# Performance work log

Hardware: AMD Instinct MI355X
Metric: run time of the kernel (lower is better)

## Reference

```python
import jax, jax.numpy as jnp
import numpy as np

N = 50000
E = 800000
IN_DIM = 128
HID = 128
OUT_DIM = 64


def _xavier(key, fan_in, fan_out):
    # matches nn.init.xavier_uniform_ on a (out, in) weight
    limit = float(np.sqrt(6.0 / (fan_in + fan_out)))
    return jax.random.uniform(key, (fan_in, fan_out), jnp.float32, -limit, limit)


def setup_inputs() -> dict:
    key = jax.random.key(0)
    ks = jax.random.split(key, 7)
    X = jax.random.normal(ks[0], (N, IN_DIM), jnp.float32)
    edge_row = jax.random.randint(ks[1], (E,), 0, N, jnp.int32)
    edge_col = jax.random.randint(ks[2], (E,), 0, N, jnp.int32)
    edge_weight = jax.random.uniform(ks[3], (E,), jnp.float32)
    W1 = _xavier(ks[4], IN_DIM, HID)
    b1 = jnp.zeros((HID,), jnp.float32)
    W2 = _xavier(ks[5], HID, HID)
    b2 = jnp.zeros((HID,), jnp.float32)
    W3 = _xavier(ks[6], HID, OUT_DIM)
    b3 = jnp.zeros((OUT_DIM,), jnp.float32)
    return {"X": X, "edge_row": edge_row, "edge_col": edge_col,
            "edge_weight": edge_weight,
            "W1": W1, "b1": b1, "W2": W2, "b2": b2, "W3": W3, "b3": b3}


def _spmm(edge_row, edge_col, edge_weight, H):
    # sparse A @ H via gather + segment_sum (COO SpMM)
    msgs = edge_weight[:, None] * H[edge_col]  # [E, d]
    return jax.ops.segment_sum(msgs, edge_row, num_segments=N)


def reference(X, edge_row, edge_col, edge_weight, W1, b1, W2, b2, W3, b3):
    # layer 1: SpMM -> linear -> relu (dropout disabled: eval mode)
    h = _spmm(edge_row, edge_col, edge_weight, X)
    h = jax.nn.relu(h @ W1 + b1)
    # layer 2
    h = _spmm(edge_row, edge_col, edge_weight, h)
    h = jax.nn.relu(h @ W2 + b2)
    # layer 3 (no activation)
    h = _spmm(edge_row, edge_col, edge_weight, h)
    return h @ W3 + b3
```

## Files before the change

### kernel.cpp

```cpp
#include <hip/hip_runtime.h>


typedef unsigned int uint32;
using bf16x8 = __attribute__((ext_vector_type(8))) short;
using f32x4  = __attribute__((ext_vector_type(4))) float;

static __device__ __forceinline__ unsigned short f2bf(float x) {
    unsigned int u = __builtin_bit_cast(unsigned int, x);
    u += 0x7FFFu + ((u >> 16) & 1u);
    return (unsigned short)(u >> 16);
}
static __device__ __forceinline__ float bflo(uint32 u) {
    return __builtin_bit_cast(float, u << 16);
}
static __device__ __forceinline__ float bfhi(uint32 u) {
    return __builtin_bit_cast(float, u & 0xFFFF0000u);
}


__global__ __launch_bounds__(256) void bucket_hist_kernel(const int* __restrict__ erow,
                                                          int* __restrict__ bcnt, int e) {
    __shared__ int h[512];
    int t = threadIdx.x;
    h[t] = 0; h[t + 256] = 0;
    __syncthreads();
    int base = blockIdx.x * 4096;
#pragma unroll
    for (int j = 0; j < 4; j++) {
        int idx = base + j * 1024 + t * 4;
        if (idx + 3 < e) {
            int4 r = *reinterpret_cast<const int4*>(&erow[idx]);
            atomicAdd(&h[r.x >> 7], 1); atomicAdd(&h[r.y >> 7], 1);
            atomicAdd(&h[r.z >> 7], 1); atomicAdd(&h[r.w >> 7], 1);
        } else {
            for (int q = 0; q < 4; q++) {
                int i2 = idx + q;
                if (i2 < e) atomicAdd(&h[erow[i2] >> 7], 1);
            }
        }
    }
    __syncthreads();
    if (h[t])       atomicAdd(&bcnt[t], h[t]);
    if (h[t + 256]) atomicAdd(&bcnt[t + 256], h[t + 256]);
}

__global__ __launch_bounds__(512) void bucket_scan_kernel(const int* __restrict__ bcnt,
                                                          int* __restrict__ boff,
                                                          int* __restrict__ bcur,
                                                          int* __restrict__ row_ptr,
                                                          int nb, int n) {
    __shared__ int sm[512];
    int t = threadIdx.x;
    int v = (t < nb) ? bcnt[t] : 0;
    sm[t] = v;
    __syncthreads();
    for (int off = 1; off < 512; off <<= 1) {
        int u = (t >= off) ? sm[t - off] : 0;
        __syncthreads();
        sm[t] += u;
        __syncthreads();
    }
    if (t < nb) { boff[t] = sm[t] - v; bcur[t] = sm[t] - v; }
    if (t == 511) { boff[nb] = sm[511]; row_ptr[n] = sm[511]; }
}

__global__ __launch_bounds__(256) void bucket_scatter_kernel(const int* __restrict__ erow,
                                                             const int* __restrict__ ecol,
                                                             const float* __restrict__ ew,
                                                             int* __restrict__ bcur,
                                                             int2* __restrict__ ebuf, int e) {
    __shared__ int hist[512];
    __shared__ int psc[256];
    __shared__ int fixup[512];
    __shared__ int2 stage[4096];
    int t = threadIdx.x;
    hist[t] = 0; hist[t + 256] = 0;
    __syncthreads();
    int base = blockIdx.x * 4096;
    int4 rows[4];
#pragma unroll
    for (int j = 0; j < 4; j++) {
        int idx = base + j * 1024 + t * 4;
        int4 r = make_int4(-1, -1, -1, -1);
        if (idx + 3 < e) {
            r = *reinterpret_cast<const int4*>(&erow[idx]);
        } else {
            if (idx < e)     r.x = erow[idx];
            if (idx + 1 < e) r.y = erow[idx + 1];
            if (idx + 2 < e) r.z = erow[idx + 2];
            if (idx + 3 < e) r.w = erow[idx + 3];
        }
        rows[j] = r;
        if (r.x >= 0) atomicAdd(&hist[r.x >> 7], 1);
        if (r.y >= 0) atomicAdd(&hist[r.y >> 7], 1);
        if (r.z >= 0) atomicAdd(&hist[r.z >> 7], 1);
        if (r.w >= 0) atomicAdd(&hist[r.w >> 7], 1);
    }
    __syncthreads();
    int c0 = hist[2 * t], c1 = hist[2 * t + 1];
    int s = c0 + c1;
    psc[t] = s;
    __syncthreads();
    for (int off = 1; off < 256; off <<= 1) {
        int u = (t >= off) ? psc[t - off] : 0;
        __syncthreads();
        psc[t] += u;
        __syncthreads();
    }
    int lo0 = psc[t] - s;
    int lo1 = lo0 + c0;
    if (c0) fixup[2 * t]     = atomicAdd(&bcur[2 * t], c0) - lo0;
    if (c1) fixup[2 * t + 1] = atomicAdd(&bcur[2 * t + 1], c1) - lo1;
    __syncthreads();
    hist[2 * t] = lo0; hist[2 * t + 1] = lo1;
    __syncthreads();
#pragma unroll
    for (int j = 0; j < 4; j++) {
        int idx = base + j * 1024 + t * 4;
        int4 r = rows[j];
        int4 c = make_int4(0, 0, 0, 0);
        float4 w = make_float4(0.f, 0.f, 0.f, 0.f);
        if (idx + 3 < e) {
            c = *reinterpret_cast<const int4*>(&ecol[idx]);
            w = *reinterpret_cast<const float4*>(&ew[idx]);
        } else {
            if (idx < e)     { c.x = ecol[idx];     w.x = ew[idx]; }
            if (idx + 1 < e) { c.y = ecol[idx + 1]; w.y = ew[idx + 1]; }
            if (idx + 2 < e) { c.z = ecol[idx + 2]; w.z = ew[idx + 2]; }
            if (idx + 3 < e) { c.w = ecol[idx + 3]; w.w = ew[idx + 3]; }
        }
        if (r.x >= 0) { int b = r.x >> 7; int sl = atomicAdd(&hist[b], 1);
            stage[sl] = make_int2((b << 23) | ((r.x & 127) << 16) | c.x, __builtin_bit_cast(int, w.x)); }
        if (r.y >= 0) { int b = r.y >> 7; int sl = atomicAdd(&hist[b], 1);
            stage[sl] = make_int2((b << 23) | ((r.y & 127) << 16) | c.y, __builtin_bit_cast(int, w.y)); }
        if (r.z >= 0) { int b = r.z >> 7; int sl = atomicAdd(&hist[b], 1);
            stage[sl] = make_int2((b << 23) | ((r.z & 127) << 16) | c.z, __builtin_bit_cast(int, w.z)); }
        if (r.w >= 0) { int b = r.w >> 7; int sl = atomicAdd(&hist[b], 1);
            stage[sl] = make_int2((b << 23) | ((r.w & 127) << 16) | c.w, __builtin_bit_cast(int, w.w)); }
    }
    __syncthreads();
    int ecnt = min(4096, e - base);
    for (int i = t; i < ecnt; i += 256) {
        int2 v = stage[i];
        int b = ((unsigned)v.x) >> 23;
        ebuf[fixup[b] + i] = v;
    }
}

__global__ __launch_bounds__(256) void bucket_sort_kernel(const int* __restrict__ boff,
                                                          const int2* __restrict__ ebuf,
                                                          int2* __restrict__ ecsr,
                                                          int* __restrict__ row_ptr, int n) {
    constexpr int MAXB = 3072;
    int b = blockIdx.x;
    int off = boff[b];
    int cnt = min(boff[b + 1] - off, MAXB);
    __shared__ int2 stage[MAXB];
    __shared__ int2 sorted[MAXB];
    __shared__ int rc[128], rs[128], c2[128];
    int t = threadIdx.x;
    if (t < 128) { rc[t] = 0; c2[t] = 0; }
    __syncthreads();
    for (int i = t; i < cnt; i += 256) {
        int2 v = ebuf[off + i];
        stage[i] = v;
        atomicAdd(&rc[(v.x >> 16) & 127], 1);
    }
    __syncthreads();
    if (t < 128) rs[t] = rc[t];
    __syncthreads();
    for (int o = 1; o < 128; o <<= 1) {
        int u = 0;
        if (t < 128 && t >= o) u = rs[t - o];
        __syncthreads();
        if (t < 128) rs[t] += u;
        __syncthreads();
    }
    if (t < 128) {
        int gr = b * 128 + t;
        if (gr < n) row_ptr[gr] = off + rs[t] - rc[t];
    }
    __syncthreads();
    for (int i = t; i < cnt; i += 256) {
        int2 v = stage[i];
        int r = (v.x >> 16) & 127;
        int pos = rs[r] - rc[r] + atomicAdd(&c2[r], 1);
        sorted[pos] = make_int2(v.x & 0xFFFF, v.y);
    }
    __syncthreads();
    for (int i = t; i < cnt; i += 256) ecsr[off + i] = sorted[i];
}

__global__ __launch_bounds__(256) void transpose_w_kernel(const float* __restrict__ W,
                                                          unsigned short* __restrict__ Wt,
                                                          int N) {
    int gid = blockIdx.x * 256 + threadIdx.x;
    int k = gid & 127;
    int nn = gid >> 7;
    Wt[gid] = f2bf(W[k * N + nn]);
}

template <bool AF32, int NOUT>
__global__ __launch_bounds__(256) void gemm_mfma_kernel(const void* __restrict__ Ap,
                                                        const unsigned short* __restrict__ Wt,
                                                        unsigned short* __restrict__ Zb, int n) {
    constexpr int CT = NOUT / 16;
    int wave = threadIdx.x >> 6;
    int lane = threadIdx.x & 63;
    int m0 = blockIdx.x * 64 + wave * 16;
    int r = lane & 15;
    int g = lane >> 4;
    int arow = min(m0 + r, n - 1);
    f32x4 acc[CT] = {};
#pragma unroll
    for (int kt = 0; kt < 4; kt++) {
        int k0 = kt * 32 + g * 8;
        bf16x8 a;
        if constexpr (AF32) {
            const float* A = (const float*)Ap;
            float4 x0 = *reinterpret_cast<const float4*>(&A[(size_t)arow * 128 + k0]);
            float4 x1 = *reinterpret_cast<const float4*>(&A[(size_t)arow * 128 + k0 + 4]);
            a[0] = (short)f2bf(x0.x); a[1] = (short)f2bf(x0.y);
            a[2] = (short)f2bf(x0.z); a[3] = (short)f2bf(x0.w);
            a[4] = (short)f2bf(x1.x); a[5] = (short)f2bf(x1.y);
            a[6] = (short)f2bf(x1.z); a[7] = (short)f2bf(x1.w);
        } else {
            const unsigned short* A = (const unsigned short*)Ap;
            a = *reinterpret_cast<const bf16x8*>(&A[(size_t)arow * 128 + k0]);
        }
#pragma unroll
        for (int c = 0; c < CT; c++) {
            bf16x8 bb = *reinterpret_cast<const bf16x8*>(&Wt[(size_t)(c * 16 + r) * 128 + k0]);
            acc[c] = __builtin_amdgcn_mfma_f32_16x16x32_bf16(a, bb, acc[c], 0, 0, 0);
        }
    }
#pragma unroll
    for (int c = 0; c < CT; c++) {
#pragma unroll
        for (int rr = 0; rr < 4; rr++) {
            int row = m0 + g * 4 + rr;
            if (row < n) Zb[(size_t)row * NOUT + c * 16 + r] = f2bf(acc[c][rr]);
        }
    }
}

__global__ __launch_bounds__(256) void spmm128_kernel(const int* __restrict__ row_ptr,
                                                      const int2* __restrict__ ecw,
                                                      const unsigned short* __restrict__ Zb,
                                                      const float* __restrict__ bias,
                                                      unsigned short* __restrict__ Hb, int n) {
    int row = (blockIdx.x * blockDim.x + threadIdx.x) >> 6;
    int lane = threadIdx.x & 63;
    if (row >= n) return;
    int beg = row_ptr[row], end = row_ptr[row + 1];
    const int grp = lane >> 4;
    const int gl  = lane & 15;
    float acc[8] = {0.f, 0.f, 0.f, 0.f, 0.f, 0.f, 0.f, 0.f};
#pragma unroll 2
    for (int k0 = beg; k0 < end; k0 += 4) {
        int k = k0 + grp;
        bool valid = (k < end);
        int kc = valid ? k : (end - 1);
        int2 cw = ecw[kc];
        float w = valid ? __builtin_bit_cast(float, cw.y) : 0.f;
        uint4 z = *reinterpret_cast<const uint4*>(&Zb[((size_t)(uint32)cw.x << 7) + (gl << 3)]);
        acc[0] = fmaf(w, bflo(z.x), acc[0]);
        acc[1] = fmaf(w, bfhi(z.x), acc[1]);
        acc[2] = fmaf(w, bflo(z.y), acc[2]);
        acc[3] = fmaf(w, bfhi(z.y), acc[3]);
        acc[4] = fmaf(w, bflo(z.z), acc[4]);
        acc[5] = fmaf(w, bfhi(z.z), acc[5]);
        acc[6] = fmaf(w, bflo(z.w), acc[6]);
        acc[7] = fmaf(w, bfhi(z.w), acc[7]);
    }
#pragma unroll
    for (int j = 0; j < 8; j++) {
        acc[j] += __shfl_xor(acc[j], 16, 64);
        acc[j] += __shfl_xor(acc[j], 32, 64);
    }
    if (lane < 16) {
        int d0 = gl << 3;
        float4 b0 = *reinterpret_cast<const float4*>(&bias[d0]);
        float4 b1 = *reinterpret_cast<const float4*>(&bias[d0 + 4]);
        float v0 = fmaxf(acc[0] + b0.x, 0.f), v1 = fmaxf(acc[1] + b0.y, 0.f);
        float v2 = fmaxf(acc[2] + b0.z, 0.f), v3 = fmaxf(acc[3] + b0.w, 0.f);
        float v4 = fmaxf(acc[4] + b1.x, 0.f), v5 = fmaxf(acc[5] + b1.y, 0.f);
        float v6 = fmaxf(acc[6] + b1.z, 0.f), v7 = fmaxf(acc[7] + b1.w, 0.f);
        uint4 pk;
        pk.x = (uint32)f2bf(v0) | ((uint32)f2bf(v1) << 16);
        pk.y = (uint32)f2bf(v2) | ((uint32)f2bf(v3) << 16);
        pk.z = (uint32)f2bf(v4) | ((uint32)f2bf(v5) << 16);
        pk.w = (uint32)f2bf(v6) | ((uint32)f2bf(v7) << 16);
        *reinterpret_cast<uint4*>(&Hb[(size_t)row * 128 + d0]) = pk;
    }
}

__global__ __launch_bounds__(256) void spmm64_kernel(const int* __restrict__ row_ptr,
                                                     const int2* __restrict__ ecw,
                                                     const unsigned short* __restrict__ Zb,
                                                     const float* __restrict__ bias,
                                                     float* __restrict__ out, int n) {
    int row = (blockIdx.x * blockDim.x + threadIdx.x) >> 6;
    int lane = threadIdx.x & 63;
    if (row >= n) return;
    int beg = row_ptr[row], end = row_ptr[row + 1];
    const int grp = lane >> 4;
    const int gl  = lane & 15;
    float acc[4] = {0.f, 0.f, 0.f, 0.f};
#pragma unroll 2
    for (int k0 = beg; k0 < end; k0 += 4) {
        int k = k0 + grp;
        bool valid = (k < end);
        int kc = valid ? k : (end - 1);
        int2 cw = ecw[kc];
        float w = valid ? __builtin_bit_cast(float, cw.y) : 0.f;
        uint2 z = *reinterpret_cast<const uint2*>(&Zb[((size_t)(uint32)cw.x << 6) + (gl << 2)]);
        acc[0] = fmaf(w, bflo(z.x), acc[0]);
        acc[1] = fmaf(w, bfhi(z.x), acc[1]);
        acc[2] = fmaf(w, bflo(z.y), acc[2]);
        acc[3] = fmaf(w, bfhi(z.y), acc[3]);
    }
#pragma unroll
    for (int j = 0; j < 4; j++) {
        acc[j] += __shfl_xor(acc[j], 16, 64);
        acc[j] += __shfl_xor(acc[j], 32, 64);
    }
    if (lane < 16) {
        int d0 = gl << 2;
        float4 b0 = *reinterpret_cast<const float4*>(&bias[d0]);
        float4 v0 = make_float4(acc[0] + b0.x, acc[1] + b0.y, acc[2] + b0.z, acc[3] + b0.w);
        *reinterpret_cast<float4*>(&out[(size_t)row * 64 + d0]) = v0;
    }
}

extern "C" void kernel_launch(void* const* d_in, const int* in_sizes, int n_in,
                              void* d_out, int out_size, void* d_ws, size_t ws_size,
                              hipStream_t stream) {
    const float* X    = (const float*)d_in[0];
    const int*   erow = (const int*)d_in[1];
    const int*   ecol = (const int*)d_in[2];
    const float* ew   = (const float*)d_in[3];
    const float* W1   = (const float*)d_in[4];
    const float* b1   = (const float*)d_in[5];
    const float* W2   = (const float*)d_in[6];
    const float* b2   = (const float*)d_in[7];
    const float* W3   = (const float*)d_in[8];
    const float* b3   = (const float*)d_in[9];
    float* out = (float*)d_out;

    const int n = in_sizes[0] / 128;
    const int e = in_sizes[1];
    const int nb = (n + 127) >> 7;

    char* p = (char*)d_ws;
    auto alloc = [&](size_t bytes) {
        void* r = (void*)p;
        p += (bytes + 255) & ~(size_t)255;
        return r;
    };
    int*            row_ptr = (int*)alloc((size_t)(n + 1) * sizeof(int));
    int*            bcnt    = (int*)alloc((size_t)nb * sizeof(int));
    int*            boff    = (int*)alloc((size_t)(nb + 1) * sizeof(int));
    int*            bcur    = (int*)alloc((size_t)nb * sizeof(int));
    int2*           ebuf    = (int2*)alloc((size_t)e * sizeof(int2));
    int2*           ecsr    = (int2*)alloc((size_t)e * sizeof(int2));
    unsigned short* Zb      = (unsigned short*)alloc((size_t)n * 128 * sizeof(unsigned short));
    unsigned short* Hb      = (unsigned short*)alloc((size_t)n * 128 * sizeof(unsigned short));
    unsigned short* Wt1     = (unsigned short*)alloc(128 * 128 * sizeof(unsigned short));
    unsigned short* Wt2     = (unsigned short*)alloc(128 * 128 * sizeof(unsigned short));
    unsigned short* Wt3     = (unsigned short*)alloc(64 * 128 * sizeof(unsigned short));

    const int eb4k = (e + 4095) / 4096;
    const int gemm_grid = (n + 63) / 64;
    const int spmm_grid = (n + 3) / 4;

    hipMemsetAsync(bcnt, 0, (size_t)nb * sizeof(int), stream);
    bucket_hist_kernel<<<eb4k, 256, 0, stream>>>(erow, bcnt, e);
    bucket_scan_kernel<<<1, 512, 0, stream>>>(bcnt, boff, bcur, row_ptr, nb, n);
    bucket_scatter_kernel<<<eb4k, 256, 0, stream>>>(erow, ecol, ew, bcur, ebuf, e);
    bucket_sort_kernel<<<nb, 256, 0, stream>>>(boff, ebuf, ecsr, row_ptr, n);

    transpose_w_kernel<<<64, 256, 0, stream>>>(W1, Wt1, 128);
    transpose_w_kernel<<<64, 256, 0, stream>>>(W2, Wt2, 128);
    transpose_w_kernel<<<32, 256, 0, stream>>>(W3, Wt3, 64);

    gemm_mfma_kernel<true, 128><<<gemm_grid, 256, 0, stream>>>(X, Wt1, Zb, n);
    spmm128_kernel<<<spmm_grid, 256, 0, stream>>>(row_ptr, ecsr, Zb, b1, Hb, n);

    gemm_mfma_kernel<false, 128><<<gemm_grid, 256, 0, stream>>>(Hb, Wt2, Zb, n);
    spmm128_kernel<<<spmm_grid, 256, 0, stream>>>(row_ptr, ecsr, Zb, b2, Hb, n);

    gemm_mfma_kernel<false, 64><<<gemm_grid, 256, 0, stream>>>(Hb, Wt3, Zb, n);
    spmm64_kernel<<<spmm_grid, 256, 0, stream>>>(row_ptr, ecsr, Zb, b3, out, n);
}
```

Measured before the change: 194.2 us.

## Drop histogram pass with fixed-capacity buckets, fuse prep, and restructure SpMM lanes

Removes the histogram and scan kernels by scattering edges into fixed-capacity per-bucket slots (BCAP=3072). The bucket sort kernel now computes bucket offsets itself with a redundant in-block scan. The three weight transposes and the bucket-counter reset are fused into one prep kernel, which cuts the number of launches and the memset. Both SpMM kernels are rewritten. spmm128 now has each lane own two feature columns and walk the row serially with a 4-way unroll, with no cross-lane reduction. spmm64 packs two rows per wavefront. The risks are silently dropped edges if any bucket exceeds BCAP, more serial latency per row in SpMM, and a larger scratch buffer.

```diff
diff --git a/kernel.cpp b/kernel.cpp
--- a/kernel.cpp
+++ b/kernel.cpp
@@ -4,6 +4,8 @@
 typedef unsigned int uint32;
 using bf16x8 = __attribute__((ext_vector_type(8))) short;
 using f32x4  = __attribute__((ext_vector_type(4))) float;
+
+static constexpr int BCAP = 3072;
 
 static __device__ __forceinline__ unsigned short f2bf(float x) {
     unsigned int u = __builtin_bit_cast(unsigned int, x);
@@ -17,51 +19,24 @@
     return __builtin_bit_cast(float, u & 0xFFFF0000u);
 }
 
-
-__global__ __launch_bounds__(256) void bucket_hist_kernel(const int* __restrict__ erow,
-                                                          int* __restrict__ bcnt, int e) {
-    __shared__ int h[512];
-    int t = threadIdx.x;
-    h[t] = 0; h[t + 256] = 0;
-    __syncthreads();
-    int base = blockIdx.x * 4096;
-#pragma unroll
-    for (int j = 0; j < 4; j++) {
-        int idx = base + j * 1024 + t * 4;
-        if (idx + 3 < e) {
-            int4 r = *reinterpret_cast<const int4*>(&erow[idx]);
-            atomicAdd(&h[r.x >> 7], 1); atomicAdd(&h[r.y >> 7], 1);
-            atomicAdd(&h[r.z >> 7], 1); atomicAdd(&h[r.w >> 7], 1);
-        } else {
-            for (int q = 0; q < 4; q++) {
-                int i2 = idx + q;
-                if (i2 < e) atomicAdd(&h[erow[i2] >> 7], 1);
-            }
-        }
-    }
-    __syncthreads();
-    if (h[t])       atomicAdd(&bcnt[t], h[t]);
-    if (h[t + 256]) atomicAdd(&bcnt[t + 256], h[t + 256]);
-}
-
-__global__ __launch_bounds__(512) void bucket_scan_kernel(const int* __restrict__ bcnt,
-                                                          int* __restrict__ boff,
-                                                          int* __restrict__ bcur,
-                                                          int* __restrict__ row_ptr,
-                                                          int nb, int n) {
-    __shared__ int sm[512];
-    int t = threadIdx.x;
-    int v = (t < nb) ? bcnt[t] : 0;
-    sm[t] = v;
-    __syncthreads();
-    for (int off = 1; off < 512; off <<= 1) {
-        int u = (t >= off) ? sm[t - off] : 0;
-        __syncthreads();
-        sm[t] += u;
-        __syncthreads();
-    }
-    if (t < nb) { boff[t] = sm[t] - v; bcur[t] = sm[t] - v; }
-    if (t == 511) { boff[nb] = sm[511]; row_ptr[n] = sm[511]; }
+__global__ __launch_bounds__(256) void prep_kernel(const float* __restrict__ W1,
+                                                   const float* __restrict__ W2,
+                                                   const float* __restrict__ W3,
+                                                   unsigned short* __restrict__ Wt1,
+                                                   unsigned short* __restrict__ Wt2,
+                                                   unsigned short* __restrict__ Wt3,
+                                                   int* __restrict__ bcur, int nb) {
+    int gid = blockIdx.x * 256 + threadIdx.x;
+    if (gid < nb) bcur[gid] = 0;
+    if (gid < 16384) {
+        Wt1[gid] = f2bf(W1[(gid & 127) * 128 + (gid >> 7)]);
+    } else if (gid < 32768) {
+        int g = gid - 16384;
+        Wt2[g] = f2bf(W2[(g & 127) * 128 + (g >> 7)]);
+    } else if (gid < 40960) {
+        int g = gid - 32768;
+        Wt3[g] = f2bf(W3[(g & 127) * 64 + (g >> 7)]);
+    }
 }
 
 __global__ __launch_bounds__(256) void bucket_scatter_kernel(const int* __restrict__ erow,
@@ -109,8 +84,8 @@
     }
     int lo0 = psc[t] - s;
     int lo1 = lo0 + c0;
-    if (c0) fixup[2 * t]     = atomicAdd(&bcur[2 * t], c0) - lo0;
-    if (c1) fixup[2 * t + 1] = atomicAdd(&bcur[2 * t + 1], c1) - lo1;
+    if (c0) fixup[2 * t]     = 2 * t * BCAP       + atomicAdd(&bcur[2 * t], c0)     - lo0;
+    if (c1) fixup[2 * t + 1] = (2 * t + 1) * BCAP + atomicAdd(&bcur[2 * t + 1], c1) - lo1;
     __syncthreads();
     hist[2 * t] = lo0; hist[2 * t + 1] = lo1;
     __syncthreads();
@@ -143,26 +118,38 @@
     for (int i = t; i < ecnt; i += 256) {
         int2 v = stage[i];
         int b = ((unsigned)v.x) >> 23;
-        ebuf[fixup[b] + i] = v;
-    }
-}
-
-__global__ __launch_bounds__(256) void bucket_sort_kernel(const int* __restrict__ boff,
+        int gpos = fixup[b] + i;
+        if (gpos - b * BCAP < BCAP) ebuf[gpos] = v;
+    }
+}
+
+__global__ __launch_bounds__(256) void bucket_sort_kernel(const int* __restrict__ bcur,
                                                           const int2* __restrict__ ebuf,
                                                           int2* __restrict__ ecsr,
-                                                          int* __restrict__ row_ptr, int n) {
-    constexpr int MAXB = 3072;
+                                                          int* __restrict__ row_ptr,
+                                                          int n, int nb) {
+    __shared__ int sc[512];
+    __shared__ int2 stage[BCAP];
+    __shared__ int2 sorted[BCAP];
+    __shared__ int rc[128], rs[128], c2[128];
     int b = blockIdx.x;
-    int off = boff[b];
-    int cnt = min(boff[b + 1] - off, MAXB);
-    __shared__ int2 stage[MAXB];
-    __shared__ int2 sorted[MAXB];
-    __shared__ int rc[128], rs[128], c2[128];
     int t = threadIdx.x;
+    sc[t]       = (t < nb)       ? min(bcur[t], BCAP)       : 0;
+    sc[t + 256] = (t + 256 < nb) ? min(bcur[t + 256], BCAP) : 0;
     if (t < 128) { rc[t] = 0; c2[t] = 0; }
     __syncthreads();
+    for (int off = 1; off < 512; off <<= 1) {
+        int a0 = (t >= off) ? sc[t - off] : 0;
+        int a1 = (t + 256 >= off) ? sc[t + 256 - off] : 0;
+        __syncthreads();
+        sc[t] += a0; sc[t + 256] += a1;
+        __syncthreads();
+    }
+    int off_b = (b == 0) ? 0 : sc[b - 1];
+    int cnt = sc[b] - off_b;
+    if (b == 0 && t == 0) row_ptr[n] = sc[nb - 1];
     for (int i = t; i < cnt; i += 256) {
-        int2 v = ebuf[off + i];
+        int2 v = ebuf[b * BCAP + i];
         stage[i] = v;
         atomicAdd(&rc[(v.x >> 16) & 127], 1);
     }
@@ -178,7 +165,7 @@
     }
     if (t < 128) {
         int gr = b * 128 + t;
-        if (gr < n) row_ptr[gr] = off + rs[t] - rc[t];
+        if (gr < n) row_ptr[gr] = off_b + rs[t] - rc[t];
     }
     __syncthreads();
     for (int i = t; i < cnt; i += 256) {
@@ -188,16 +175,7 @@
         sorted[pos] = make_int2(v.x & 0xFFFF, v.y);
     }
     __syncthreads();
-    for (int i = t; i < cnt; i += 256) ecsr[off + i] = sorted[i];
-}
-
-__global__ __launch_bounds__(256) void transpose_w_kernel(const float* __restrict__ W,
-                                                          unsigned short* __restrict__ Wt,
-                                                          int N) {
-    int gid = blockIdx.x * 256 + threadIdx.x;
-    int k = gid & 127;
-    int nn = gid >> 7;
-    Wt[gid] = f2bf(W[k * N + nn]);
+    for (int i = t; i < cnt; i += 256) ecsr[off_b + i] = sorted[i];
 }
 
 template <bool AF32, int NOUT>
@@ -249,87 +227,83 @@
                                                       const unsigned short* __restrict__ Zb,
                                                       const float* __restrict__ bias,
                                                       unsigned short* __restrict__ Hb, int n) {
-    int row = (blockIdx.x * blockDim.x + threadIdx.x) >> 6;
+    int row = (blockIdx.x * 256 + threadIdx.x) >> 6;
     int lane = threadIdx.x & 63;
     if (row >= n) return;
-    int beg = row_ptr[row], end = row_ptr[row + 1];
-    const int grp = lane >> 4;
-    const int gl  = lane & 15;
-    float acc[8] = {0.f, 0.f, 0.f, 0.f, 0.f, 0.f, 0.f, 0.f};
-#pragma unroll 2
-    for (int k0 = beg; k0 < end; k0 += 4) {
-        int k = k0 + grp;
-        bool valid = (k < end);
-        int kc = valid ? k : (end - 1);
-        int2 cw = ecw[kc];
-        float w = valid ? __builtin_bit_cast(float, cw.y) : 0.f;
-        uint4 z = *reinterpret_cast<const uint4*>(&Zb[((size_t)(uint32)cw.x << 7) + (gl << 3)]);
-        acc[0] = fmaf(w, bflo(z.x), acc[0]);
-        acc[1] = fmaf(w, bfhi(z.x), acc[1]);
-        acc[2] = fmaf(w, bflo(z.y), acc[2]);
-        acc[3] = fmaf(w, bfhi(z.y), acc[3]);
-        acc[4] = fmaf(w, bflo(z.z), acc[4]);
-        acc[5] = fmaf(w, bfhi(z.z), acc[5]);
-        acc[6] = fmaf(w, bflo(z.w), acc[6]);
-        acc[7] = fmaf(w, bfhi(z.w), acc[7]);
-    }
-#pragma unroll
-    for (int j = 0; j < 8; j++) {
-        acc[j] += __shfl_xor(acc[j], 16, 64);
-        acc[j] += __shfl_xor(acc[j], 32, 64);
-    }
-    if (lane < 16) {
-        int d0 = gl << 3;
-        float4 b0 = *reinterpret_cast<const float4*>(&bias[d0]);
-        float4 b1 = *reinterpret_cast<const float4*>(&bias[d0 + 4]);
-        float v0 = fmaxf(acc[0] + b0.x, 0.f), v1 = fmaxf(acc[1] + b0.y, 0.f);
-        float v2 = fmaxf(acc[2] + b0.z, 0.f), v3 = fmaxf(acc[3] + b0.w, 0.f);
-        float v4 = fmaxf(acc[4] + b1.x, 0.f), v5 = fmaxf(acc[5] + b1.y, 0.f);
-        float v6 = fmaxf(acc[6] + b1.z, 0.f), v7 = fmaxf(acc[7] + b1.w, 0.f);
-        uint4 pk;
-        pk.x = (uint32)f2bf(v0) | ((uint32)f2bf(v1) << 16);
-        pk.y = (uint32)f2bf(v2) | ((uint32)f2bf(v3) << 16);
-        pk.z = (uint32)f2bf(v4) | ((uint32)f2bf(v5) << 16);
-        pk.w = (uint32)f2bf(v6) | ((uint32)f2bf(v7) << 16);
-        *reinterpret_cast<uint4*>(&Hb[(size_t)row * 128 + d0]) = pk;
-    }
+    int beg = __builtin_amdgcn_readfirstlane(row_ptr[row]);
+    int end = __builtin_amdgcn_readfirstlane(row_ptr[row + 1]);
+    int deg = end - beg;
+    const unsigned short* zb = Zb + (lane << 1);
+    float a0 = 0.f, a1 = 0.f;
+    int i = 0;
+    for (; i + 4 <= deg; i += 4) {
+        int2 e0 = ecw[beg + i];
+        int2 e1 = ecw[beg + i + 1];
+        int2 e2 = ecw[beg + i + 2];
+        int2 e3 = ecw[beg + i + 3];
+        uint32 z0 = *reinterpret_cast<const uint32*>(zb + ((size_t)(uint32)e0.x << 7));
+        uint32 z1 = *reinterpret_cast<const uint32*>(zb + ((size_t)(uint32)e1.x << 7));
+        uint32 z2 = *reinterpret_cast<const uint32*>(zb + ((size_t)(uint32)e2.x << 7));
+        uint32 z3 = *reinterpret_cast<const uint32*>(zb + ((size_t)(uint32)e3.x << 7));
+        float w0 = __builtin_bit_cast(float, e0.y);
+        float w1 = __builtin_bit_cast(float, e1.y);
+        float w2 = __builtin_bit_cast(float, e2.y);
+        float w3 = __builtin_bit_cast(float, e3.y);
+        a0 = fmaf(w0, bflo(z0), a0); a1 = fmaf(w0, bfhi(z0), a1);
+        a0 = fmaf(w1, bflo(z1), a0); a1 = fmaf(w1, bfhi(z1), a1);
+        a0 = fmaf(w2, bflo(z2), a0); a1 = fmaf(w2, bfhi(z2), a1);
+        a0 = fmaf(w3, bflo(z3), a0); a1 = fmaf(w3, bfhi(z3), a1);
+    }
+    for (; i < deg; i++) {
+        int2 e = ecw[beg + i];
+        uint32 z = *reinterpret_cast<const uint32*>(zb + ((size_t)(uint32)e.x << 7));
+        float w = __builtin_bit_cast(float, e.y);
+        a0 = fmaf(w, bflo(z), a0); a1 = fmaf(w, bfhi(z), a1);
+    }
+    float2 bv = *reinterpret_cast<const float2*>(&bias[lane << 1]);
+    a0 = fmaxf(a0 + bv.x, 0.f);
+    a1 = fmaxf(a1 + bv.y, 0.f);
+    uint32 pk = (uint32)f2bf(a0) | ((uint32)f2bf(a1) << 16);
+    *reinterpret_cast<uint32*>(&Hb[(size_t)row * 128 + (lane << 1)]) = pk;
 }
 
 __global__ __launch_bounds__(256) void spmm64_kernel(const int* __restrict__ row_ptr,
                                                      const int2* __restrict__ ecw,
                                                      const unsigned short* __restrict__ Zb,
                                                      const float* __restrict__ bias,
-                                                     float* __restrict__ out, int n) {
-    int row = (blockIdx.x * blockDim.x + threadIdx.x) >> 6;
+                                                     float* __restrict__ out, int n, int e) {
+    int gw = (blockIdx.x * 256 + threadIdx.x) >> 6;
     int lane = threadIdx.x & 63;
-    if (row >= n) return;
-    int beg = row_ptr[row], end = row_ptr[row + 1];
-    const int grp = lane >> 4;
-    const int gl  = lane & 15;
-    float acc[4] = {0.f, 0.f, 0.f, 0.f};
-#pragma unroll 2
-    for (int k0 = beg; k0 < end; k0 += 4) {
-        int k = k0 + grp;
-        bool valid = (k < end);
-        int kc = valid ? k : (end - 1);
-        int2 cw = ecw[kc];
-        float w = valid ? __builtin_bit_cast(float, cw.y) : 0.f;
-        uint2 z = *reinterpret_cast<const uint2*>(&Zb[((size_t)(uint32)cw.x << 6) + (gl << 2)]);
-        acc[0] = fmaf(w, bflo(z.x), acc[0]);
-        acc[1] = fmaf(w, bfhi(z.x), acc[1]);
-        acc[2] = fmaf(w, bflo(z.y), acc[2]);
-        acc[3] = fmaf(w, bfhi(z.y), acc[3]);
-    }
-#pragma unroll
-    for (int j = 0; j < 4; j++) {
-        acc[j] += __shfl_xor(acc[j], 16, 64);
-        acc[j] += __shfl_xor(acc[j], 32, 64);
-    }
-    if (lane < 16) {
-        int d0 = gl << 2;
-        float4 b0 = *reinterpret_cast<const float4*>(&bias[d0]);
-        float4 v0 = make_float4(acc[0] + b0.x, acc[1] + b0.y, acc[2] + b0.z, acc[3] + b0.w);
-        *reinterpret_cast<float4*>(&out[(size_t)row * 64 + d0]) = v0;
+    int half = lane >> 5;
+    int hl = lane & 31;
+    int row = gw * 2 + half;
+    bool rv = (row < n);
+    int beg = 0, end = 0;
+    if (rv) { beg = row_ptr[row]; end = row_ptr[row + 1]; }
+    int beg0 = __builtin_amdgcn_readlane(beg, 0);
+    int deg0 = __builtin_amdgcn_readlane(end, 0) - beg0;
+    int beg1 = __builtin_amdgcn_readlane(beg, 32);
+    int deg1 = __builtin_amdgcn_readlane(end, 32) - beg1;
+    int mdeg = max(deg0, deg1);
+    const unsigned short* zb = Zb + (hl << 1);
+    float a0 = 0.f, a1 = 0.f;
+    for (int i = 0; i < mdeg; i++) {
+        int iA = min(beg0 + min(i, max(deg0 - 1, 0)), e - 1);
+        int iB = min(beg1 + min(i, max(deg1 - 1, 0)), e - 1);
+        int2 eA = ecw[iA];
+        int2 eB = ecw[iB];
+        float wA = (i < deg0) ? __builtin_bit_cast(float, eA.y) : 0.f;
+        float wB = (i < deg1) ? __builtin_bit_cast(float, eB.y) : 0.f;
+        int col = half ? eB.x : eA.x;
+        float w = half ? wB : wA;
+        uint32 z = *reinterpret_cast<const uint32*>(zb + ((size_t)(uint32)col << 6));
+        a0 = fmaf(w, bflo(z), a0);
+        a1 = fmaf(w, bfhi(z), a1);
+    }
+    if (rv) {
+        float2 bv = *reinterpret_cast<const float2*>(&bias[hl << 1]);
+        float2 v = make_float2(a0 + bv.x, a1 + bv.y);
+        *reinterpret_cast<float2*>(&out[(size_t)row * 64 + (hl << 1)]) = v;
     }
 }
 
@@ -359,10 +333,8 @@
         return r;
     };
     int*            row_ptr = (int*)alloc((size_t)(n + 1) * sizeof(int));
-    int*            bcnt    = (int*)alloc((size_t)nb * sizeof(int));
-    int*            boff    = (int*)alloc((size_t)(nb + 1) * sizeof(int));
     int*            bcur    = (int*)alloc((size_t)nb * sizeof(int));
-    int2*           ebuf    = (int2*)alloc((size_t)e * sizeof(int2));
+    int2*           ebuf    = (int2*)alloc((size_t)nb * BCAP * sizeof(int2));
     int2*           ecsr    = (int2*)alloc((size_t)e * sizeof(int2));
     unsigned short* Zb      = (unsigned short*)alloc((size_t)n * 128 * sizeof(unsigned short));
     unsigned short* Hb      = (unsigned short*)alloc((size_t)n * 128 * sizeof(unsigned short));
@@ -372,24 +344,19 @@
 
     const int eb4k = (e + 4095) / 4096;
     const int gemm_grid = (n + 63) / 64;
-    const int spmm_grid = (n + 3) / 4;
-
-    hipMemsetAsync(bcnt, 0, (size_t)nb * sizeof(int), stream);
-    bucket_hist_kernel<<<eb4k, 256, 0, stream>>>(erow, bcnt, e);
-    bucket_scan_kernel<<<1, 512, 0, stream>>>(bcnt, boff, bcur, row_ptr, nb, n);
+    const int sp128_grid = (n + 3) / 4;
+    const int sp64_grid  = ((n + 1) / 2 + 3) / 4;
+
+    prep_kernel<<<160, 256, 0, stream>>>(W1, W2, W3, Wt1, Wt2, Wt3, bcur, nb);
     bucket_scatter_kernel<<<eb4k, 256, 0, stream>>>(erow, ecol, ew, bcur, ebuf, e);
-    bucket_sort_kernel<<<nb, 256, 0, stream>>>(boff, ebuf, ecsr, row_ptr, n);
-
-    transpose_w_kernel<<<64, 256, 0, stream>>>(W1, Wt1, 128);
-    transpose_w_kernel<<<64, 256, 0, stream>>>(W2, Wt2, 128);
-    transpose_w_kernel<<<32, 256, 0, stream>>>(W3, Wt3, 64);
+    bucket_sort_kernel<<<nb, 256, 0, stream>>>(bcur, ebuf, ecsr, row_ptr, n, nb);
 
     gemm_mfma_kernel<true, 128><<<gemm_grid, 256, 0, stream>>>(X, Wt1, Zb, n);
-    spmm128_kernel<<<spmm_grid, 256, 0, stream>>>(row_ptr, ecsr, Zb, b1, Hb, n);
+    spmm128_kernel<<<sp128_grid, 256, 0, stream>>>(row_ptr, ecsr, Zb, b1, Hb, n);
 
     gemm_mfma_kernel<false, 128><<<gemm_grid, 256, 0, stream>>>(Hb, Wt2, Zb, n);
-    spmm128_kernel<<<spmm_grid, 256, 0, stream>>>(row_ptr, ecsr, Zb, b2, Hb, n);
+    spmm128_kernel<<<sp128_grid, 256, 0, stream>>>(row_ptr, ecsr, Zb, b2, Hb, n);
 
     gemm_mfma_kernel<false, 64><<<gemm_grid, 256, 0, stream>>>(Hb, Wt3, Zb, n);
-    spmm64_kernel<<<spmm_grid, 256, 0, stream>>>(row_ptr, ecsr, Zb, b3, out, n);
-}
+    spmm64_kernel<<<sp64_grid, 256, 0, stream>>>(row_ptr, ecsr, Zb, b3, out, n, e);
+}
```

After: 196.0 us. No clear change (+0.9%).
